# Optimization experiments

Measured on AMD Instinct MI355X. Metric: run time of the kernel, lower is better.

## Reference

```python
import jax, jax.numpy as jnp
import numpy as np
import math

SIZE = (60, 270, 480)           # full video T, H, W
CHANNELS = 14                   # sum of per-level grid channels 8+4+2
GRID_SIZES = [(60, 16, 16, 8), (30, 8, 8, 4), (15, 4, 4, 2)]
IDX_MAX = (60, 3, 5)            # patch grid -> patch_size (1, 90, 96)
PADDING = (0, 1, 1)
N_PATCH = 64
MANIP_LBASE = 2.0
MANIP_LEVELS = 8
INIT_SCALE = 1e-3


def setup_inputs() -> dict:
    key = jax.random.key(0)
    kt, kh, kw = jax.random.split(key, 3)
    idx = jnp.stack([
        jax.random.randint(kt, (N_PATCH,), 0, IDX_MAX[0]),
        jax.random.randint(kh, (N_PATCH,), 0, IDX_MAX[1]),
        jax.random.randint(kw, (N_PATCH,), 0, IDX_MAX[2]),
    ], axis=1).astype(jnp.int32)
    inp = {
        "idx": idx,
        "idx_max": jnp.asarray(IDX_MAX, dtype=jnp.int32),
        "padding": jnp.asarray(PADDING, dtype=jnp.int32),
    }
    for i, (T, H, W, C) in enumerate(GRID_SIZES):
        k = jax.random.fold_in(key, 10 + i)
        inp[f"grid{i}"] = jax.random.normal(k, (T * H * W, C), jnp.float32) * INIT_SCALE
    return inp


def _pixel_idx_1d(ix, size_d, nmax_d, pad_d):
    # ix: [N] patch index along one dim -> ([N, P+2*pad] clipped pixel idx, mask)
    p = size_d // nmax_d
    offs = jnp.arange(-pad_d, p + pad_d)
    raw = ix[:, None] * p + offs[None, :]
    mask = ((raw >= 0) & (raw < size_d)).astype(jnp.float32)
    return jnp.clip(raw, 0, size_d - 1), mask


def reference(idx, idx_max, padding, grid0, grid1, grid2):
    T, H, W = SIZE
    im = tuple(int(v) for v in np.asarray(idx_max))
    pad = tuple(int(v) for v in np.asarray(padding))
    patch = tuple(SIZE[d] // im[d] for d in range(3))
    ppad = tuple(patch[d] + 2 * pad[d] for d in range(3))

    # Multi-level grids -> trilinear upsample to full (T,H,W,C_i), concat on C.
    # jax.image.resize 'trilinear' uses half-pixel centers == torch align_corners=False.
    enc_splits = []
    for g, (Tg, Hg, Wg, Cg) in zip((grid0, grid1, grid2), GRID_SIZES):
        enc_splits.append(jax.image.resize(g.reshape(Tg, Hg, Wg, Cg), (T, H, W, Cg), method="trilinear"))
    enc = jnp.concatenate(enc_splits, axis=-1).reshape(T * H * W, CHANNELS)

    it, mt = _pixel_idx_1d(idx[:, 0], T, im[0], pad[0])
    ih, mh = _pixel_idx_1d(idx[:, 1], H, im[1], pad[1])
    iw, mw = _pixel_idx_1d(idx[:, 2], W, im[2], pad[2])

    flat = (it[:, :, None, None] * (H * W) + ih[:, None, :, None] * W + iw[:, None, None, :]).reshape(-1)
    mask = (mt[:, :, None, None] * mh[:, None, :, None] * mw[:, None, None, :]).reshape(-1, 1)

    t_embed = (mask * enc[flat]).reshape((idx.shape[0],) + ppad + (CHANNELS,))

    bases = (MANIP_LBASE ** jnp.arange(MANIP_LEVELS, dtype=jnp.float32)) * math.pi
    v = idx[:, 0].astype(jnp.float32)[:, None] * bases
    t_manip = jnp.concatenate([jnp.sin(v), jnp.cos(v)], axis=-1)  # [N, 2*levels]

    return t_embed, t_manip
```

## Files before the change

kernel.cpp:

```cpp
#include <hip/hip_runtime.h>
#include <math.h>


#define N_PATCH 64
#define PPAD_H 92
#define PPAD_W 98
#define CH 14
#define PIX_PER_PATCH (PPAD_H * PPAD_W)
#define ROWS_PER_BLOCK 12
#define BLOCKS_PER_PATCH 8
#define ELEMS_PER_PATCH (PIX_PER_PATCH * CH)
#define ELEMS_PER_ROW (PPAD_W * CH)
#define F4_PER_CHUNK (2 * ELEMS_PER_ROW / 4)
#define TOTAL_EMBED (N_PATCH * ELEMS_PER_PATCH)
#define TOTAL_MANIP (N_PATCH * 16)

#define RB_STRIDE 72
#define L1_OFF 48
#define L2_OFF 64
#define V_ENTRIES (ROWS_PER_BLOCK * 70)

__device__ __forceinline__ float lerpf(float a, float b, float f) {
    return a + f * (b - a);
}

__device__ __forceinline__ int wcell0(int rw0, float sw, int Wg) {
    float x = ((float)rw0 + 0.5f) * sw - 0.5f;
    int w0 = (int)floorf(x);
    return min(max(w0, 0), Wg - 1);
}

__global__ __launch_bounds__(256) void embed_kernel(
    const int* __restrict__ idx,
    const float* __restrict__ g0,
    const float* __restrict__ g1,
    const float* __restrict__ g2,
    float* __restrict__ out)
{
    __shared__ __align__(16) float s_V[ROWS_PER_BLOCK * RB_STRIDE];
    __shared__ float4 s_wl[3][PPAD_W];
    __shared__ __align__(16) float s_bufA[2 * ELEMS_PER_ROW];
    __shared__ __align__(16) float s_bufB[2 * ELEMS_PER_ROW];

    const int tid = threadIdx.x;
    const int bx  = blockIdx.x;
    const int n   = blockIdx.y;
    const int it  = idx[3 * n + 0];
    const int ih  = idx[3 * n + 1];
    const int iw  = idx[3 * n + 2];
    const int rw0 = iw * 96 - 1;
    const int row0 = bx * ROWS_PER_BLOCK;

    const float sw0 = (float)((double)16 / 480.0);
    const float sw1 = (float)((double)8  / 480.0);
    const float sw2 = (float)((double)4  / 480.0);
    const float sh0 = (float)((double)16 / 270.0);
    const float sh1 = (float)((double)8  / 270.0);
    const float sh2 = (float)((double)4  / 270.0);

    if (bx == 0 && n == 0) {
        float* om = out + TOTAL_EMBED;
        for (int e = tid; e < TOTAL_MANIP; e += 256) {
            int nn = e >> 4;
            int j  = e & 15;
            int l  = j & 7;
            float base = (float)M_PI * (float)(1 << l);
            float v = (float)idx[3 * nn + 0] * base;
            double dv = (double)v;
            om[e] = (float)((j < 8) ? sin(dv) : cos(dv));
        }
    }

    const int C0_0 = wcell0(rw0, sw0, 16);
    const int C0_1 = wcell0(rw0, sw1, 8);
    const int C0_2 = wcell0(rw0, sw2, 4);
    for (int e = tid; e < V_ENTRIES; e += 256) {
        int row = e / 70;
        int off = e - 70 * row;
        int rh  = ih * 90 + row0 + row - 1;
        float mh = ((unsigned)rh < 270u) ? 1.0f : 0.0f;
        float v;
        if (off < L1_OFF) {
            int cell = off >> 3, chn = off & 7;
            float xh = ((float)rh + 0.5f) * sh0 - 0.5f;
            float ff = floorf(xh);
            float fh = xh - ff;
            int h0 = (int)ff;
            int h0c = min(max(h0, 0), 15), h1c = min(h0 + 1, 15);
            int cw = min(C0_0 + cell, 15);
            const float* base = g0 + (size_t)it * 2048;
            float a = base[(h0c * 16 + cw) * 8 + chn];
            float b = base[(h1c * 16 + cw) * 8 + chn];
            v = mh * lerpf(a, b, fh);
        } else if (off < L2_OFF) {
            int o = off - L1_OFF;
            int cell = o >> 2, chn = o & 3;
            float xh = ((float)rh + 0.5f) * sh1 - 0.5f;
            float ff = floorf(xh);
            float fh = xh - ff;
            int h0 = (int)ff;
            int h0c = min(max(h0, 0), 7), h1c = min(h0 + 1, 7);
            float xt = ((float)it + 0.5f) * 0.5f - 0.5f;
            float ftf = floorf(xt);
            float ft  = xt - ftf;
            int t0 = (int)ftf;
            int t0c = min(max(t0, 0), 29), t1c = min(t0 + 1, 29);
            int cw = min(C0_1 + cell, 7);
            float a00 = g1[((t0c * 8 + h0c) * 8 + cw) * 4 + chn];
            float a01 = g1[((t0c * 8 + h1c) * 8 + cw) * 4 + chn];
            float a10 = g1[((t1c * 8 + h0c) * 8 + cw) * 4 + chn];
            float a11 = g1[((t1c * 8 + h1c) * 8 + cw) * 4 + chn];
            v = mh * lerpf(lerpf(a00, a01, fh), lerpf(a10, a11, fh), ft);
        } else {
            int o = off - L2_OFF;
            int cell = o >> 1, chn = o & 1;
            float xh = ((float)rh + 0.5f) * sh2 - 0.5f;
            float ff = floorf(xh);
            float fh = xh - ff;
            int h0 = (int)ff;
            int h0c = min(max(h0, 0), 3), h1c = min(h0 + 1, 3);
            float xt = ((float)it + 0.5f) * 0.25f - 0.5f;
            float ftf = floorf(xt);
            float ft  = xt - ftf;
            int t0 = (int)ftf;
            int t0c = min(max(t0, 0), 14), t1c = min(t0 + 1, 14);
            int cw = min(C0_2 + cell, 3);
            float a00 = g2[((t0c * 4 + h0c) * 4 + cw) * 2 + chn];
            float a01 = g2[((t0c * 4 + h1c) * 4 + cw) * 2 + chn];
            float a10 = g2[((t1c * 4 + h0c) * 4 + cw) * 2 + chn];
            float a11 = g2[((t1c * 4 + h1c) * 4 + cw) * 2 + chn];
            v = mh * lerpf(lerpf(a00, a01, fh), lerpf(a10, a11, fh), ft);
        }
        s_V[row * RB_STRIDE + off] = v;
    }

    for (int i = tid; i < 3 * PPAD_W; i += 256) {
        int lvl = (i >= PPAD_W) + (i >= 2 * PPAD_W);
        int ww  = i - PPAD_W * lvl;
        int Wg  = (lvl == 0) ? 16 : ((lvl == 1) ? 8 : 4);
        int cs  = (lvl == 0) ? 8  : ((lvl == 1) ? 4 : 2);
        int bb  = (lvl == 0) ? 0  : ((lvl == 1) ? L1_OFF : L2_OFF);
        int C0  = (lvl == 0) ? C0_0 : ((lvl == 1) ? C0_1 : C0_2);
        float sw = (lvl == 0) ? sw0 : ((lvl == 1) ? sw1 : sw2);
        int rw = iw * 96 + ww - 1;
        float mask = ((unsigned)rw < 480u) ? 1.0f : 0.0f;
        float x  = ((float)rw + 0.5f) * sw - 0.5f;
        float ff = floorf(x);
        float f  = x - ff;
        int w0 = (int)ff;
        int wa = min(max(w0, 0), Wg - 1);
        int wb = min(w0 + 1, Wg - 1);
        s_wl[lvl][ww] = make_float4(__int_as_float(bb + (wa - C0) * cs),
                                    __int_as_float(bb + (wb - C0) * cs), f, mask);
    }

    __syncthreads();

    const bool active = tid < 2 * PPAD_W;
    int par = 0, oA0 = 0, oB0 = 0, oA1 = 0, oB1 = 0, oA2 = 0, oB2 = 0;
    float fw0 = 0.f, fw1 = 0.f, fw2 = 0.f, mw = 0.f;
    if (active) {
        par = tid >= PPAD_W;
        int ww = tid - PPAD_W * par;
        float4 wl0 = s_wl[0][ww];
        float4 wl1 = s_wl[1][ww];
        float4 wl2 = s_wl[2][ww];
        oA0 = __float_as_int(wl0.x); oB0 = __float_as_int(wl0.y); fw0 = wl0.z;
        oA1 = __float_as_int(wl1.x); oB1 = __float_as_int(wl1.y); fw1 = wl1.z;
        oA2 = __float_as_int(wl2.x); oB2 = __float_as_int(wl2.y); fw2 = wl2.z;
        mw  = wl0.w;
    }

    const int nrows   = min(ROWS_PER_BLOCK, PPAD_H - row0);
    const int nchunks = nrows >> 1;
    float* outp = out + (size_t)n * ELEMS_PER_PATCH;

    auto compute_chunk = [&](int c, float* __restrict__ buf) {
        if (!active) return;
        const float* V = s_V + (2 * c + par) * RB_STRIDE;
        float4 A0 = *(const float4*)(V + oA0);
        float4 A1 = *(const float4*)(V + oA0 + 4);
        float4 B0 = *(const float4*)(V + oB0);
        float4 B1 = *(const float4*)(V + oB0 + 4);
        float4 C1a = *(const float4*)(V + oA1);
        float4 C1b = *(const float4*)(V + oB1);
        float2 C2a = *(const float2*)(V + oA2);
        float2 C2b = *(const float2*)(V + oB2);
        float r0  = mw * lerpf(A0.x, B0.x, fw0);
        float r1  = mw * lerpf(A0.y, B0.y, fw0);
        float r2  = mw * lerpf(A0.z, B0.z, fw0);
        float r3  = mw * lerpf(A0.w, B0.w, fw0);
        float r4  = mw * lerpf(A1.x, B1.x, fw0);
        float r5  = mw * lerpf(A1.y, B1.y, fw0);
        float r6  = mw * lerpf(A1.z, B1.z, fw0);
        float r7  = mw * lerpf(A1.w, B1.w, fw0);
        float r8  = mw * lerpf(C1a.x, C1b.x, fw1);
        float r9  = mw * lerpf(C1a.y, C1b.y, fw1);
        float r10 = mw * lerpf(C1a.z, C1b.z, fw1);
        float r11 = mw * lerpf(C1a.w, C1b.w, fw1);
        float r12 = mw * lerpf(C2a.x, C2b.x, fw2);
        float r13 = mw * lerpf(C2a.y, C2b.y, fw2);
        float2* b = (float2*)(buf + tid * CH);
        b[0] = make_float2(r0,  r1);
        b[1] = make_float2(r2,  r3);
        b[2] = make_float2(r4,  r5);
        b[3] = make_float2(r6,  r7);
        b[4] = make_float2(r8,  r9);
        b[5] = make_float2(r10, r11);
        b[6] = make_float2(r12, r13);
    };

    compute_chunk(0, s_bufA);
    __syncthreads();
    for (int c = 1; c < nchunks; ++c) {
        float* prev = (c & 1) ? s_bufA : s_bufB;
        float* cur  = (c & 1) ? s_bufB : s_bufA;
        const float4* sb = (const float4*)prev;
        float4* gb = (float4*)(outp + (size_t)(row0 + 2 * (c - 1)) * ELEMS_PER_ROW);
        for (int j = tid; j < F4_PER_CHUNK; j += 256) gb[j] = sb[j];
        compute_chunk(c, cur);
        __syncthreads();
    }
    {
        float* last = ((nchunks - 1) & 1) ? s_bufB : s_bufA;
        const float4* sb = (const float4*)last;
        float4* gb = (float4*)(outp + (size_t)(row0 + 2 * (nchunks - 1)) * ELEMS_PER_ROW);
        for (int j = tid; j < F4_PER_CHUNK; j += 256) gb[j] = sb[j];
    }
}

extern "C" void kernel_launch(void* const* d_in, const int* in_sizes, int n_in,
                              void* d_out, int out_size, void* d_ws, size_t ws_size,
                              hipStream_t stream) {
    const int*   idx = (const int*)  d_in[0];
    const float* g0  = (const float*)d_in[3];
    const float* g1  = (const float*)d_in[4];
    const float* g2  = (const float*)d_in[5];
    float* out = (float*)d_out;

    dim3 grid(BLOCKS_PER_PATCH, N_PATCH);
    embed_kernel<<<grid, 256, 0, stream>>>(idx, g0, g1, g2, out);
}
```

Measured before the change: 15.02 us.

## Assign one row per wavefront with wave-local staging, more blocks per patch

Each block now covers 4 output rows instead of 12, so there are 23 blocks per patch instead of 8. Each 64-lane wavefront owns one row and computes it in two 64-pixel halves. Results are staged in a wave-private LDS buffer and synchronised only with wave barriers and explicit lgkmcnt waits, which replaces the block-wide __syncthreads double buffering. The aim is more parallelism across CUs and no block-level sync on the write path. The cost is more redundant per-block setup, such as loading grid rows and building the weight tables, across the larger number of blocks.

Result: faster. 13.60 us (-9.5%).

```diff
diff --git a/kernel.cpp b/kernel.cpp
--- a/kernel.cpp
+++ b/kernel.cpp
@@ -6,12 +6,10 @@
 #define PPAD_H 92
 #define PPAD_W 98
 #define CH 14
-#define PIX_PER_PATCH (PPAD_H * PPAD_W)
-#define ROWS_PER_BLOCK 12
-#define BLOCKS_PER_PATCH 8
-#define ELEMS_PER_PATCH (PIX_PER_PATCH * CH)
+#define ROWS_PER_BLOCK 4
+#define BLOCKS_PER_PATCH 23
 #define ELEMS_PER_ROW (PPAD_W * CH)
-#define F4_PER_CHUNK (2 * ELEMS_PER_ROW / 4)
+#define ELEMS_PER_PATCH (PPAD_H * ELEMS_PER_ROW)
 #define TOTAL_EMBED (N_PATCH * ELEMS_PER_PATCH)
 #define TOTAL_MANIP (N_PATCH * 16)
 
@@ -39,8 +37,7 @@
 {
     __shared__ __align__(16) float s_V[ROWS_PER_BLOCK * RB_STRIDE];
     __shared__ float4 s_wl[3][PPAD_W];
-    __shared__ __align__(16) float s_bufA[2 * ELEMS_PER_ROW];
-    __shared__ __align__(16) float s_bufB[2 * ELEMS_PER_ROW];
+    __shared__ __align__(16) float s_buf[4 * 64 * CH];
 
     const int tid = threadIdx.x;
     const int bx  = blockIdx.x;
@@ -156,76 +153,62 @@
 
     __syncthreads();
 
-    const bool active = tid < 2 * PPAD_W;
-    int par = 0, oA0 = 0, oB0 = 0, oA1 = 0, oB1 = 0, oA2 = 0, oB2 = 0;
-    float fw0 = 0.f, fw1 = 0.f, fw2 = 0.f, mw = 0.f;
-    if (active) {
-        par = tid >= PPAD_W;
-        int ww = tid - PPAD_W * par;
-        float4 wl0 = s_wl[0][ww];
-        float4 wl1 = s_wl[1][ww];
-        float4 wl2 = s_wl[2][ww];
-        oA0 = __float_as_int(wl0.x); oB0 = __float_as_int(wl0.y); fw0 = wl0.z;
-        oA1 = __float_as_int(wl1.x); oB1 = __float_as_int(wl1.y); fw1 = wl1.z;
-        oA2 = __float_as_int(wl2.x); oB2 = __float_as_int(wl2.y); fw2 = wl2.z;
-        mw  = wl0.w;
-    }
-
-    const int nrows   = min(ROWS_PER_BLOCK, PPAD_H - row0);
-    const int nchunks = nrows >> 1;
-    float* outp = out + (size_t)n * ELEMS_PER_PATCH;
-
-    auto compute_chunk = [&](int c, float* __restrict__ buf) {
-        if (!active) return;
-        const float* V = s_V + (2 * c + par) * RB_STRIDE;
-        float4 A0 = *(const float4*)(V + oA0);
-        float4 A1 = *(const float4*)(V + oA0 + 4);
-        float4 B0 = *(const float4*)(V + oB0);
-        float4 B1 = *(const float4*)(V + oB0 + 4);
-        float4 C1a = *(const float4*)(V + oA1);
-        float4 C1b = *(const float4*)(V + oB1);
-        float2 C2a = *(const float2*)(V + oA2);
-        float2 C2b = *(const float2*)(V + oB2);
-        float r0  = mw * lerpf(A0.x, B0.x, fw0);
-        float r1  = mw * lerpf(A0.y, B0.y, fw0);
-        float r2  = mw * lerpf(A0.z, B0.z, fw0);
-        float r3  = mw * lerpf(A0.w, B0.w, fw0);
-        float r4  = mw * lerpf(A1.x, B1.x, fw0);
-        float r5  = mw * lerpf(A1.y, B1.y, fw0);
-        float r6  = mw * lerpf(A1.z, B1.z, fw0);
-        float r7  = mw * lerpf(A1.w, B1.w, fw0);
-        float r8  = mw * lerpf(C1a.x, C1b.x, fw1);
-        float r9  = mw * lerpf(C1a.y, C1b.y, fw1);
-        float r10 = mw * lerpf(C1a.z, C1b.z, fw1);
-        float r11 = mw * lerpf(C1a.w, C1b.w, fw1);
-        float r12 = mw * lerpf(C2a.x, C2b.x, fw2);
-        float r13 = mw * lerpf(C2a.y, C2b.y, fw2);
-        float2* b = (float2*)(buf + tid * CH);
-        b[0] = make_float2(r0,  r1);
-        b[1] = make_float2(r2,  r3);
-        b[2] = make_float2(r4,  r5);
-        b[3] = make_float2(r6,  r7);
-        b[4] = make_float2(r8,  r9);
-        b[5] = make_float2(r10, r11);
-        b[6] = make_float2(r12, r13);
-    };
-
-    compute_chunk(0, s_bufA);
-    __syncthreads();
-    for (int c = 1; c < nchunks; ++c) {
-        float* prev = (c & 1) ? s_bufA : s_bufB;
-        float* cur  = (c & 1) ? s_bufB : s_bufA;
-        const float4* sb = (const float4*)prev;
-        float4* gb = (float4*)(outp + (size_t)(row0 + 2 * (c - 1)) * ELEMS_PER_ROW);
-        for (int j = tid; j < F4_PER_CHUNK; j += 256) gb[j] = sb[j];
-        compute_chunk(c, cur);
-        __syncthreads();
-    }
-    {
-        float* last = ((nchunks - 1) & 1) ? s_bufB : s_bufA;
-        const float4* sb = (const float4*)last;
-        float4* gb = (float4*)(outp + (size_t)(row0 + 2 * (nchunks - 1)) * ELEMS_PER_ROW);
-        for (int j = tid; j < F4_PER_CHUNK; j += 256) gb[j] = sb[j];
+    const int wv   = tid >> 6;
+    const int lane = tid & 63;
+    float* lbuf = s_buf + wv * (64 * CH);
+    const float* V = s_V + wv * RB_STRIDE;
+    float* orow = out + (size_t)n * ELEMS_PER_PATCH
+                      + (size_t)(row0 + wv) * ELEMS_PER_ROW;
+
+    #pragma unroll
+    for (int s = 0; s < 2; ++s) {
+        asm volatile("s_waitcnt lgkmcnt(0)" ::: "memory");
+        __builtin_amdgcn_sched_barrier(0);
+        int ww = s * 64 + lane;
+        if (ww < PPAD_W) {
+            float4 wl0 = s_wl[0][ww];
+            float4 wl1 = s_wl[1][ww];
+            float4 wl2 = s_wl[2][ww];
+            int oA0 = __float_as_int(wl0.x), oB0 = __float_as_int(wl0.y);
+            int oA1 = __float_as_int(wl1.x), oB1 = __float_as_int(wl1.y);
+            int oA2 = __float_as_int(wl2.x), oB2 = __float_as_int(wl2.y);
+            float fw0 = wl0.z, fw1 = wl1.z, fw2 = wl2.z, mw = wl0.w;
+
+            float4 A0  = *(const float4*)(V + oA0);
+            float4 A1  = *(const float4*)(V + oA0 + 4);
+            float4 B0  = *(const float4*)(V + oB0);
+            float4 B1  = *(const float4*)(V + oB0 + 4);
+            float4 C1a = *(const float4*)(V + oA1);
+            float4 C1b = *(const float4*)(V + oB1);
+            float2 C2a = *(const float2*)(V + oA2);
+            float2 C2b = *(const float2*)(V + oB2);
+
+            float2* b = (float2*)(lbuf + lane * CH);
+            b[0] = make_float2(mw * lerpf(A0.x, B0.x, fw0),
+                               mw * lerpf(A0.y, B0.y, fw0));
+            b[1] = make_float2(mw * lerpf(A0.z, B0.z, fw0),
+                               mw * lerpf(A0.w, B0.w, fw0));
+            b[2] = make_float2(mw * lerpf(A1.x, B1.x, fw0),
+                               mw * lerpf(A1.y, B1.y, fw0));
+            b[3] = make_float2(mw * lerpf(A1.z, B1.z, fw0),
+                               mw * lerpf(A1.w, B1.w, fw0));
+            b[4] = make_float2(mw * lerpf(C1a.x, C1b.x, fw1),
+                               mw * lerpf(C1a.y, C1b.y, fw1));
+            b[5] = make_float2(mw * lerpf(C1a.z, C1b.z, fw1),
+                               mw * lerpf(C1a.w, C1b.w, fw1));
+            b[6] = make_float2(mw * lerpf(C2a.x, C2b.x, fw2),
+                               mw * lerpf(C2a.y, C2b.y, fw2));
+        }
+        __builtin_amdgcn_wave_barrier();
+        asm volatile("s_waitcnt lgkmcnt(0)" ::: "memory");
+        __builtin_amdgcn_sched_barrier(0);
+
+        const int npx = (s == 0) ? 64 : (PPAD_W - 64);
+        const int nf4 = npx * CH / 4;
+        const float4* sb = (const float4*)lbuf;
+        float4* gb = (float4*)(orow + s * 64 * CH);
+        for (int j = lane; j < nf4; j += 64) gb[j] = sb[j];
+        __builtin_amdgcn_wave_barrier();
     }
 }
 
```
